# Kernel tuning notes

Hardware: AMD Instinct MI355X
Metric: run time of the kernel (lower is better)

Reference implementation:

```python
import jax, jax.numpy as jnp
import numpy as np

N, F_IN, F_OUT = 8192, 256, 128
ALPHA = 0.2  # LeakyReLU negative slope
NEG_INF = -9e15


def setup_inputs() -> dict:
    key = jax.random.key(0)
    k1, k2, k3, k4 = jax.random.split(key, 4)
    h = jax.random.normal(k1, (N, F_IN), dtype=jnp.float32)
    adj = jax.random.randint(k2, (N, N), 0, 2, dtype=jnp.int32)
    # Xavier-uniform-like init (gain=1.414)
    lim_w = 1.414 * np.sqrt(6.0 / (F_IN + F_OUT))
    W = jax.random.uniform(k3, (F_IN, F_OUT), dtype=jnp.float32, minval=-lim_w, maxval=lim_w)
    lim_a = 1.414 * np.sqrt(6.0 / (2 * F_OUT + 1))
    a = jax.random.uniform(k4, (2 * F_OUT, 1), dtype=jnp.float32, minval=-lim_a, maxval=lim_a)
    return {"h": h, "adj": adj, "W": W, "a": a}


def reference(h, adj, W, a):
    # Wh: [N, F_OUT]
    Wh = h @ W
    f_out = W.shape[1]
    # The torch code builds an [N, N, 2F] concat tensor; mathematically
    # e_ij = leakyrelu(a1 . Wh_i + a2 . Wh_j), so compute via two projections.
    a1 = a[:f_out, 0]   # [F_OUT]
    a2 = a[f_out:, 0]   # [F_OUT]
    f1 = Wh @ a1        # [N]
    f2 = Wh @ a2        # [N]
    e = jax.nn.leaky_relu(f1[:, None] + f2[None, :], negative_slope=ALPHA)  # [N, N]
    e = jnp.where(adj > 0, e, NEG_INF)
    attention = jax.nn.softmax(e, axis=1)  # [N, N]; dropout p=0 (eval mode)
    h_prime = attention @ Wh               # [N, F_OUT]
    return jax.nn.elu(h_prime)
```

## Files before the change

kernel.cpp:

```cpp
#include <hip/hip_runtime.h>
#include <hip/hip_bf16.h>
#include <math.h>

typedef short short8 __attribute__((ext_vector_type(8)));
typedef float f32x4 __attribute__((ext_vector_type(4)));
typedef int i32x4 __attribute__((ext_vector_type(4)));

#define NN 8192
#define FIN 256
#define FOUT 128
#define LRELU_A 0.2f
#define L2E 1.44269504088896f

__device__ __forceinline__ short f2bf(float x) {
    unsigned u = __builtin_bit_cast(unsigned, x);
    unsigned r = (u + 0x7FFFu + ((u >> 16) & 1u)) >> 16;
    return (short)r;
}

__device__ __forceinline__ short f2bf_fast(float x) {
    return __builtin_bit_cast(short, __float2bfloat16(x));
}

__global__ __launch_bounds__(256) void k_pack(const int* __restrict__ adj,
                                              unsigned* __restrict__ packed) {
    __shared__ unsigned char nib[2048];
    const int row = blockIdx.x;
    const int tid = threadIdx.x;
    const i32x4* base = (const i32x4*)(adj + (size_t)row * NN);
    #pragma unroll
    for (int q = 0; q < 8; ++q) {
        int idx = q * 256 + tid;
        i32x4 v = __builtin_nontemporal_load(base + idx);
        unsigned b = (unsigned)(v.x & 1)        | ((unsigned)(v.y & 1) << 1) |
                     ((unsigned)(v.z & 1) << 2) | ((unsigned)(v.w & 1) << 3);
        nib[idx] = (unsigned char)b;
    }
    __syncthreads();
    unsigned long long n8 = *(const unsigned long long*)&nib[tid * 8];
    unsigned w = 0;
    #pragma unroll
    for (int j = 0; j < 8; ++j)
        w |= ((unsigned)((n8 >> (8 * j)) & 0xFull)) << (4 * j);
    packed[(size_t)row * (NN / 32) + tid] = w;
}

__global__ __launch_bounds__(256) void k_wh(const float* __restrict__ h,
                                            const float* __restrict__ W,
                                            const float* __restrict__ a,
                                            short* __restrict__ WhT,
                                            float* __restrict__ f1,
                                            float* __restrict__ f2) {
    __shared__ float hs[8][FIN];
    const int tid = threadIdx.x;
    const int r0 = blockIdx.x * 8;
    #pragma unroll
    for (int i = 0; i < 2; ++i) {
        int f4 = tid + 256 * i;
        int row = f4 >> 6;
        int k4 = (f4 & 63) << 2;
        *(float4*)&hs[row][k4] = *(const float4*)(h + (size_t)(r0 + row) * FIN + k4);
    }
    __syncthreads();
    const int c4 = (tid & 31) * 4;
    const int row = tid >> 5;
    float acc0 = 0.f, acc1 = 0.f, acc2 = 0.f, acc3 = 0.f;
    #pragma unroll 4
    for (int k = 0; k < FIN; ++k) {
        float hv = hs[row][k];
        float4 w4 = *(const float4*)(W + (size_t)k * FOUT + c4);
        acc0 = fmaf(hv, w4.x, acc0);
        acc1 = fmaf(hv, w4.y, acc1);
        acc2 = fmaf(hv, w4.z, acc2);
        acc3 = fmaf(hv, w4.w, acc3);
    }
    const int wr = r0 + row;
    WhT[(size_t)(c4 + 0) * NN + wr] = f2bf(acc0);
    WhT[(size_t)(c4 + 1) * NN + wr] = f2bf(acc1);
    WhT[(size_t)(c4 + 2) * NN + wr] = f2bf(acc2);
    WhT[(size_t)(c4 + 3) * NN + wr] = f2bf(acc3);

    float4 a1v = *(const float4*)(a + c4);
    float4 a2v = *(const float4*)(a + FOUT + c4);
    float p1 = acc0 * a1v.x + acc1 * a1v.y + acc2 * a1v.z + acc3 * a1v.w;
    float p2 = acc0 * a2v.x + acc1 * a2v.y + acc2 * a2v.z + acc3 * a2v.w;
    #pragma unroll
    for (int m = 1; m <= 16; m <<= 1) {
        p1 += __shfl_xor(p1, m, 64);
        p2 += __shfl_xor(p2, m, 64);
    }
    if ((tid & 31) == 0) {
        f1[wr] = p1;
        f2[wr] = p2;
    }
}

__global__ __launch_bounds__(256) void k_gmax(const float* __restrict__ f2,
                                              float* __restrict__ gmax) {
    const int tid = threadIdx.x;
    float m = -1e30f;
    for (int i = tid; i < NN; i += 256) m = fmaxf(m, f2[i]);
    #pragma unroll
    for (int s = 1; s <= 32; s <<= 1) m = fmaxf(m, __shfl_xor(m, s, 64));
    __shared__ float red[4];
    if ((tid & 63) == 0) red[tid >> 6] = m;
    __syncthreads();
    if (tid == 0) gmax[0] = fmaxf(fmaxf(red[0], red[1]), fmaxf(red[2], red[3]));
}

__device__ __forceinline__ void gat_body(const short* __restrict__ lrd, unsigned m8,
                                         float4 fa, float4 fb,
                                         float c1, float c2,
                                         f32x4 acc[9], short8 ones) {
    short8 b0 = *(const short8*)(lrd + 0 * 1024);
    short8 b1 = *(const short8*)(lrd + 1 * 1024);
    short8 b2 = *(const short8*)(lrd + 2 * 1024);
    short8 b3 = *(const short8*)(lrd + 3 * 1024);
    short8 b4 = *(const short8*)(lrd + 4 * 1024);
    short8 b5 = *(const short8*)(lrd + 5 * 1024);
    short8 b6 = *(const short8*)(lrd + 6 * 1024);
    short8 b7 = *(const short8*)(lrd + 7 * 1024);

    float fv[8] = {fa.x, fa.y, fa.z, fa.w, fb.x, fb.y, fb.z, fb.w};
    short8 af;
    #pragma unroll
    for (int i = 0; i < 8; ++i) {
        float u = fv[i] + c1;
        float v = fmaf(LRELU_A, fv[i], c2);
        float p = __builtin_amdgcn_exp2f(fmaxf(u, v));
        p = (m8 & (1u << i)) ? p : 0.0f;
        af[i] = f2bf_fast(p);
    }
    acc[0] = __builtin_amdgcn_mfma_f32_16x16x32_bf16(af, b0, acc[0], 0, 0, 0);
    acc[1] = __builtin_amdgcn_mfma_f32_16x16x32_bf16(af, b1, acc[1], 0, 0, 0);
    acc[2] = __builtin_amdgcn_mfma_f32_16x16x32_bf16(af, b2, acc[2], 0, 0, 0);
    acc[3] = __builtin_amdgcn_mfma_f32_16x16x32_bf16(af, b3, acc[3], 0, 0, 0);
    acc[4] = __builtin_amdgcn_mfma_f32_16x16x32_bf16(af, b4, acc[4], 0, 0, 0);
    acc[5] = __builtin_amdgcn_mfma_f32_16x16x32_bf16(af, b5, acc[5], 0, 0, 0);
    acc[6] = __builtin_amdgcn_mfma_f32_16x16x32_bf16(af, b6, acc[6], 0, 0, 0);
    acc[7] = __builtin_amdgcn_mfma_f32_16x16x32_bf16(af, b7, acc[7], 0, 0, 0);
    acc[8] = __builtin_amdgcn_mfma_f32_16x16x32_bf16(af, ones, acc[8], 0, 0, 0);
}

#define GAT_STEP(KOFF, MC, LRD0, LRD1, BUFW)                                       \
    {                                                                              \
        const int koff_ = (KOFF);                                                  \
        float4 fa0 = *(const float4*)(lf2 + koff_);                                \
        float4 fb0 = *(const float4*)(lf2 + koff_ + 4);                            \
        float4 fa1 = *(const float4*)(lf2 + koff_ + 32);                           \
        float4 fb1 = *(const float4*)(lf2 + koff_ + 36);                           \
        unsigned m0 = (MC.x >> mshift) & 0xffu;                                    \
        unsigned m1 = (MC.y >> mshift) & 0xffu;                                    \
        const int kpm_ = (koff_ + 128 < kchunk) ? koff_ + 128 : 0;                 \
        MC = *(const uint2*)(pkrow + (kpm_ >> 5));                                 \
        const int kst_ = (koff_ + 64 < kchunk) ? koff_ + 64 : 0;                   \
        short8 r0 = *(const short8*)(g00 + kst_);                                  \
        short8 r1 = *(const short8*)(g01 + kst_);                                  \
        short8 r2 = *(const short8*)(g10 + kst_);                                  \
        short8 r3 = *(const short8*)(g11 + kst_);                                  \
        gat_body(LRD0, m0, fa0, fb0, c1, c2, acc, ones);                           \
        gat_body(LRD1, m1, fa1, fb1, c1, c2, acc, ones);                           \
        *(short8*)((BUFW) + d00) = r0;                                             \
        *(short8*)((BUFW) + d01) = r1;                                             \
        *(short8*)((BUFW) + d10) = r2;                                             \
        *(short8*)((BUFW) + d11) = r3;                                             \
        asm volatile("s_waitcnt lgkmcnt(0)" ::: "memory");                         \
        __builtin_amdgcn_s_barrier();                                              \
    }

__global__ __launch_bounds__(256, 4) void k_attn(const unsigned* __restrict__ packed,
                                                 const short* __restrict__ WhT,
                                                 const float* __restrict__ f1,
                                                 const float* __restrict__ f2,
                                                 const float* __restrict__ gmax,
                                                 float* __restrict__ numb,
                                                 float* __restrict__ denb,
                                                 int kchunk, int nsplit) {
    __shared__ __align__(16) short ldsW[2][8192];
    __shared__ __align__(16) float ldsF2[2048];
    const int tid = threadIdx.x;
    const int lane = tid & 63;
    const int wave = tid >> 6;
    const int split = blockIdx.x & (nsplit - 1);
    const int rt = blockIdx.x / nsplit;
    const int rowbase = rt * 64 + wave * 16;
    const int col = lane & 15;
    const int kg = lane >> 4;
    const int arow = rowbase + col;

    const float f1r = f1[arow];
    const float gm = gmax[0];
    const float t0v = f1r + gm;
    const float mhat = fmaxf(t0v, LRELU_A * t0v);
    const float mh2 = mhat * L2E;
    const float c1 = fmaf(f1r, L2E, -mh2);
    const float c2 = fmaf(LRELU_A * f1r, L2E, -mh2);

    const short8 ones = {0x3F80, 0x3F80, 0x3F80, 0x3F80,
                         0x3F80, 0x3F80, 0x3F80, 0x3F80};

    const int kbase0 = split * kchunk;
    const unsigned* pkrow = packed + (size_t)arow * (NN / 32) + (kbase0 >> 5);
    const int mshift = kg * 8;
    const float* lf2 = ldsF2 + kg * 8;

    const int srow = wave * 32 + (lane >> 2);
    const int sx = srow & 7;
    const short* gsb = WhT + (size_t)srow * NN + kbase0 + (lane & 3) * 8;
    const short* g00 = gsb;
    const short* g01 = gsb + 32;
    const short* g10 = gsb + (size_t)16 * NN;
    const short* g11 = gsb + (size_t)16 * NN + 32;
    const int d00 = srow * 64        + ((((lane & 3) + 0) ^ sx) * 8);
    const int d01 = srow * 64        + ((((lane & 3) + 4) ^ sx) * 8);
    const int d10 = (srow + 16) * 64 + ((((lane & 3) + 0) ^ sx) * 8);
    const int d11 = (srow + 16) * 64 + ((((lane & 3) + 4) ^ sx) * 8);
    short* buf0 = &ldsW[0][0];
    short* buf1 = &ldsW[1][0];

    const short* lrdE0 = &ldsW[0][col * 64 + ((kg ^ (col & 7)) * 8)];
    const short* lrdE1 = &ldsW[0][col * 64 + (((kg ^ (col & 7)) * 8) ^ 32)];
    const short* lrdO0 = lrdE0 + 8192;
    const short* lrdO1 = lrdE1 + 8192;

    f32x4 acc[9] = {};

    for (int i = tid * 4; i < kchunk; i += 1024) {
        float4 v = *(const float4*)(f2 + kbase0 + i);
        v.x *= L2E; v.y *= L2E; v.z *= L2E; v.w *= L2E;
        *(float4*)&ldsF2[i] = v;
    }
    {
        short8 r0 = *(const short8*)(g00);
        short8 r1 = *(const short8*)(g01);
        short8 r2 = *(const short8*)(g10);
        short8 r3 = *(const short8*)(g11);
        *(short8*)(buf0 + d00) = r0;
        *(short8*)(buf0 + d01) = r1;
        *(short8*)(buf0 + d10) = r2;
        *(short8*)(buf0 + d11) = r3;
    }
    uint2 mA = *(const uint2*)(pkrow);
    uint2 mB = *(const uint2*)(pkrow + 2);
    asm volatile("s_waitcnt lgkmcnt(0)" ::: "memory");
    __builtin_amdgcn_s_barrier();

    for (int koff = 0; koff < kchunk; koff += 128) {
        GAT_STEP(koff,      mA, lrdE0, lrdE1, buf1);
        GAT_STEP(koff + 64, mB, lrdO0, lrdO1, buf0);
    }

    const int rsub = (lane >> 4) * 4;
    if (col == 0) {
        #pragma unroll
        for (int r = 0; r < 4; ++r)
            denb[(size_t)split * NN + rowbase + rsub + r] = acc[8][r];
    }

    float* np = numb + ((size_t)split * NN + rowbase) * FOUT;
    #pragma unroll
    for (int t = 0; t < 8; ++t) {
        #pragma unroll
        for (int r = 0; r < 4; ++r) {
            np[(size_t)(rsub + r) * FOUT + t * 16 + col] = acc[t][r];
        }
    }
}

__global__ __launch_bounds__(256) void k_final(const float* __restrict__ numb,
                                               const float* __restrict__ denb,
                                               float* __restrict__ out,
                                               int splitk) {
    const int idx = blockIdx.x * 256 + threadIdx.x;
    const int row = idx >> 7;
    float s = 0.0f, d = 0.0f;
    for (int sp = 0; sp < splitk; ++sp) {
        s += numb[((size_t)sp * NN) * FOUT + idx];
        d += denb[(size_t)sp * NN + row];
    }
    float v = s / d;
    out[idx] = v > 0.0f ? v : expm1f(v);
}

extern "C" void kernel_launch(void* const* d_in, const int* in_sizes, int n_in,
                              void* d_out, int out_size, void* d_ws, size_t ws_size,
                              hipStream_t stream) {
    const float* h = (const float*)d_in[0];
    const int* adj = (const int*)d_in[1];
    const float* W = (const float*)d_in[2];
    const float* a = (const float*)d_in[3];
    float* out = (float*)d_out;

    char* ws = (char*)d_ws;
    size_t off = 0;
    auto alloc = [&](size_t nbytes) {
        char* p = ws + off;
        off = (off + nbytes + 255) & ~(size_t)255;
        return p;
    };
    short* WhT     = (short*)alloc((size_t)FOUT * NN * 2);
    float* f1      = (float*)alloc(NN * 4);
    float* f2      = (float*)alloc(NN * 4);
    float* gmx     = (float*)alloc(256);
    unsigned* pkd  = (unsigned*)alloc((size_t)NN * (NN / 32) * 4);

    int splitk = 8;
    while (splitk > 1 &&
           off + (size_t)splitk * ((size_t)NN * FOUT * 4 + NN * 4 + 512) > ws_size)
        splitk >>= 1;
    float* numb = (float*)alloc((size_t)splitk * NN * FOUT * 4);
    float* denb = (float*)alloc((size_t)splitk * NN * 4);
    const int kchunk = NN / splitk;

    k_wh<<<NN / 8, 256, 0, stream>>>(h, W, a, WhT, f1, f2);
    k_gmax<<<1, 256, 0, stream>>>(f2, gmx);
    k_pack<<<NN, 256, 0, stream>>>(adj, pkd);
    k_attn<<<(NN / 64) * splitk, 256, 0, stream>>>(pkd, WhT, f1, f2, gmx, numb, denb,
                                                   kchunk, splitk);
    k_final<<<NN * FOUT / 256, 256, 0, stream>>>(numb, denb, out, splitk);
}
```

Measured before the change: 132.8 us.

## Compute two 16-row tiles per wave in attention and fuse Wh with adjacency packing

Each wave in the attention kernel now handles 32 rows instead of 16, so every WhT B-fragment read from LDS feeds two sets of MFMAs. That halves LDS traffic and staging per output row, at the cost of doubled accumulator registers, which is why launch bounds drop from 4 to 2 blocks per CU. The Wh projection and the adjacency bit-packing are also merged into one prep kernel, removing a launch. The split-k floor is raised to 4.

```diff
diff --git a/kernel.cpp b/kernel.cpp
--- a/kernel.cpp
+++ b/kernel.cpp
@@ -22,38 +22,19 @@
     return __builtin_bit_cast(short, __float2bfloat16(x));
 }
 
-__global__ __launch_bounds__(256) void k_pack(const int* __restrict__ adj,
+__global__ __launch_bounds__(256) void k_prep(const float* __restrict__ h,
+                                              const float* __restrict__ W,
+                                              const float* __restrict__ a,
+                                              const int* __restrict__ adj,
+                                              short* __restrict__ WhT,
+                                              float* __restrict__ f1,
+                                              float* __restrict__ f2,
                                               unsigned* __restrict__ packed) {
+    __shared__ float hs[8][FIN];
     __shared__ unsigned char nib[2048];
-    const int row = blockIdx.x;
-    const int tid = threadIdx.x;
-    const i32x4* base = (const i32x4*)(adj + (size_t)row * NN);
-    #pragma unroll
-    for (int q = 0; q < 8; ++q) {
-        int idx = q * 256 + tid;
-        i32x4 v = __builtin_nontemporal_load(base + idx);
-        unsigned b = (unsigned)(v.x & 1)        | ((unsigned)(v.y & 1) << 1) |
-                     ((unsigned)(v.z & 1) << 2) | ((unsigned)(v.w & 1) << 3);
-        nib[idx] = (unsigned char)b;
-    }
-    __syncthreads();
-    unsigned long long n8 = *(const unsigned long long*)&nib[tid * 8];
-    unsigned w = 0;
-    #pragma unroll
-    for (int j = 0; j < 8; ++j)
-        w |= ((unsigned)((n8 >> (8 * j)) & 0xFull)) << (4 * j);
-    packed[(size_t)row * (NN / 32) + tid] = w;
-}
-
-__global__ __launch_bounds__(256) void k_wh(const float* __restrict__ h,
-                                            const float* __restrict__ W,
-                                            const float* __restrict__ a,
-                                            short* __restrict__ WhT,
-                                            float* __restrict__ f1,
-                                            float* __restrict__ f2) {
-    __shared__ float hs[8][FIN];
     const int tid = threadIdx.x;
     const int r0 = blockIdx.x * 8;
+
     #pragma unroll
     for (int i = 0; i < 2; ++i) {
         int f4 = tid + 256 * i;
@@ -93,6 +74,26 @@
         f1[wr] = p1;
         f2[wr] = p2;
     }
+
+    const i32x4* abase = (const i32x4*)(adj + (size_t)r0 * NN);
+    for (int r = 0; r < 8; ++r) {
+        #pragma unroll
+        for (int q = 0; q < 8; ++q) {
+            int idx = q * 256 + tid;
+            i32x4 v = __builtin_nontemporal_load(abase + (size_t)r * 2048 + idx);
+            unsigned b = (unsigned)(v.x & 1)        | ((unsigned)(v.y & 1) << 1) |
+                         ((unsigned)(v.z & 1) << 2) | ((unsigned)(v.w & 1) << 3);
+            nib[idx] = (unsigned char)b;
+        }
+        __syncthreads();
+        unsigned long long n8 = *(const unsigned long long*)&nib[tid * 8];
+        unsigned w = 0;
+        #pragma unroll
+        for (int j = 0; j < 8; ++j)
+            w |= ((unsigned)((n8 >> (8 * j)) & 0xFull)) << (4 * j);
+        packed[(size_t)(r0 + r) * (NN / 32) + tid] = w;
+        __syncthreads();
+    }
 }
 
 __global__ __launch_bounds__(256) void k_gmax(const float* __restrict__ f2,
@@ -108,10 +109,13 @@
     if (tid == 0) gmax[0] = fmaxf(fmaxf(red[0], red[1]), fmaxf(red[2], red[3]));
 }
 
-__device__ __forceinline__ void gat_body(const short* __restrict__ lrd, unsigned m8,
-                                         float4 fa, float4 fb,
-                                         float c1, float c2,
-                                         f32x4 acc[9], short8 ones) {
+__device__ __forceinline__ void gat_body2(const short* __restrict__ lrd,
+                                          unsigned m8L, unsigned m8H,
+                                          float4 fa, float4 fb,
+                                          float c1L, float c2L,
+                                          float c1H, float c2H,
+                                          f32x4 accL[9], f32x4 accH[9],
+                                          short8 ones) {
     short8 b0 = *(const short8*)(lrd + 0 * 1024);
     short8 b1 = *(const short8*)(lrd + 1 * 1024);
     short8 b2 = *(const short8*)(lrd + 2 * 1024);
@@ -122,44 +126,63 @@
     short8 b7 = *(const short8*)(lrd + 7 * 1024);
 
     float fv[8] = {fa.x, fa.y, fa.z, fa.w, fb.x, fb.y, fb.z, fb.w};
-    short8 af;
+    short8 afL, afH;
     #pragma unroll
     for (int i = 0; i < 8; ++i) {
-        float u = fv[i] + c1;
-        float v = fmaf(LRELU_A, fv[i], c2);
+        float u = fv[i] + c1L;
+        float v = fmaf(LRELU_A, fv[i], c2L);
         float p = __builtin_amdgcn_exp2f(fmaxf(u, v));
-        p = (m8 & (1u << i)) ? p : 0.0f;
-        af[i] = f2bf_fast(p);
-    }
-    acc[0] = __builtin_amdgcn_mfma_f32_16x16x32_bf16(af, b0, acc[0], 0, 0, 0);
-    acc[1] = __builtin_amdgcn_mfma_f32_16x16x32_bf16(af, b1, acc[1], 0, 0, 0);
-    acc[2] = __builtin_amdgcn_mfma_f32_16x16x32_bf16(af, b2, acc[2], 0, 0, 0);
-    acc[3] = __builtin_amdgcn_mfma_f32_16x16x32_bf16(af, b3, acc[3], 0, 0, 0);
-    acc[4] = __builtin_amdgcn_mfma_f32_16x16x32_bf16(af, b4, acc[4], 0, 0, 0);
-    acc[5] = __builtin_amdgcn_mfma_f32_16x16x32_bf16(af, b5, acc[5], 0, 0, 0);
-    acc[6] = __builtin_amdgcn_mfma_f32_16x16x32_bf16(af, b6, acc[6], 0, 0, 0);
-    acc[7] = __builtin_amdgcn_mfma_f32_16x16x32_bf16(af, b7, acc[7], 0, 0, 0);
-    acc[8] = __builtin_amdgcn_mfma_f32_16x16x32_bf16(af, ones, acc[8], 0, 0, 0);
-}
-
-#define GAT_STEP(KOFF, MC, LRD0, LRD1, BUFW)                                       \
+        afL[i] = f2bf_fast((m8L & (1u << i)) ? p : 0.0f);
+    }
+    accL[0] = __builtin_amdgcn_mfma_f32_16x16x32_bf16(afL, b0, accL[0], 0, 0, 0);
+    accL[1] = __builtin_amdgcn_mfma_f32_16x16x32_bf16(afL, b1, accL[1], 0, 0, 0);
+    accL[2] = __builtin_amdgcn_mfma_f32_16x16x32_bf16(afL, b2, accL[2], 0, 0, 0);
+    accL[3] = __builtin_amdgcn_mfma_f32_16x16x32_bf16(afL, b3, accL[3], 0, 0, 0);
+    accL[4] = __builtin_amdgcn_mfma_f32_16x16x32_bf16(afL, b4, accL[4], 0, 0, 0);
+    accL[5] = __builtin_amdgcn_mfma_f32_16x16x32_bf16(afL, b5, accL[5], 0, 0, 0);
+    accL[6] = __builtin_amdgcn_mfma_f32_16x16x32_bf16(afL, b6, accL[6], 0, 0, 0);
+    accL[7] = __builtin_amdgcn_mfma_f32_16x16x32_bf16(afL, b7, accL[7], 0, 0, 0);
+    accL[8] = __builtin_amdgcn_mfma_f32_16x16x32_bf16(afL, ones, accL[8], 0, 0, 0);
+
+    #pragma unroll
+    for (int i = 0; i < 8; ++i) {
+        float u = fv[i] + c1H;
+        float v = fmaf(LRELU_A, fv[i], c2H);
+        float p = __builtin_amdgcn_exp2f(fmaxf(u, v));
+        afH[i] = f2bf_fast((m8H & (1u << i)) ? p : 0.0f);
+    }
+    accH[0] = __builtin_amdgcn_mfma_f32_16x16x32_bf16(afH, b0, accH[0], 0, 0, 0);
+    accH[1] = __builtin_amdgcn_mfma_f32_16x16x32_bf16(afH, b1, accH[1], 0, 0, 0);
+    accH[2] = __builtin_amdgcn_mfma_f32_16x16x32_bf16(afH, b2, accH[2], 0, 0, 0);
+    accH[3] = __builtin_amdgcn_mfma_f32_16x16x32_bf16(afH, b3, accH[3], 0, 0, 0);
+    accH[4] = __builtin_amdgcn_mfma_f32_16x16x32_bf16(afH, b4, accH[4], 0, 0, 0);
+    accH[5] = __builtin_amdgcn_mfma_f32_16x16x32_bf16(afH, b5, accH[5], 0, 0, 0);
+    accH[6] = __builtin_amdgcn_mfma_f32_16x16x32_bf16(afH, b6, accH[6], 0, 0, 0);
+    accH[7] = __builtin_amdgcn_mfma_f32_16x16x32_bf16(afH, b7, accH[7], 0, 0, 0);
+    accH[8] = __builtin_amdgcn_mfma_f32_16x16x32_bf16(afH, ones, accH[8], 0, 0, 0);
+}
+
+#define GAT_STEP(KOFF, MCL, MCH, LRD0, LRD1, BUFW)                                 \
     {                                                                              \
         const int koff_ = (KOFF);                                                  \
         float4 fa0 = *(const float4*)(lf2 + koff_);                                \
         float4 fb0 = *(const float4*)(lf2 + koff_ + 4);                            \
         float4 fa1 = *(const float4*)(lf2 + koff_ + 32);                           \
         float4 fb1 = *(const float4*)(lf2 + koff_ + 36);                           \
-        unsigned m0 = (MC.x >> mshift) & 0xffu;                                    \
-        unsigned m1 = (MC.y >> mshift) & 0xffu;                                    \
+        unsigned m0L = (MCL.x >> mshift) & 0xffu;                                  \
+        unsigned m1L = (MCL.y >> mshift) & 0xffu;                                  \
+        unsigned m0H = (MCH.x >> mshift) & 0xffu;                                  \
+        unsigned m1H = (MCH.y >> mshift) & 0xffu;                                  \
         const int kpm_ = (koff_ + 128 < kchunk) ? koff_ + 128 : 0;                 \
-        MC = *(const uint2*)(pkrow + (kpm_ >> 5));                                 \
+        MCL = *(const uint2*)(pkrowL + (kpm_ >> 5));                               \
+        MCH = *(const uint2*)(pkrowH + (kpm_ >> 5));                               \
         const int kst_ = (koff_ + 64 < kchunk) ? koff_ + 64 : 0;                   \
         short8 r0 = *(const short8*)(g00 + kst_);                                  \
         short8 r1 = *(const short8*)(g01 + kst_);                                  \
         short8 r2 = *(const short8*)(g10 + kst_);                                  \
         short8 r3 = *(const short8*)(g11 + kst_);                                  \
-        gat_body(LRD0, m0, fa0, fb0, c1, c2, acc, ones);                           \
-        gat_body(LRD1, m1, fa1, fb1, c1, c2, acc, ones);                           \
+        gat_body2(LRD0, m0L, m0H, fa0, fb0, c1L, c2L, c1H, c2H, accL, accH, ones); \
+        gat_body2(LRD1, m1L, m1H, fa1, fb1, c1L, c2L, c1H, c2H, accL, accH, ones); \
         *(short8*)((BUFW) + d00) = r0;                                             \
         *(short8*)((BUFW) + d01) = r1;                                             \
         *(short8*)((BUFW) + d10) = r2;                                             \
@@ -168,7 +191,7 @@
         __builtin_amdgcn_s_barrier();                                              \
     }
 
-__global__ __launch_bounds__(256, 4) void k_attn(const unsigned* __restrict__ packed,
+__global__ __launch_bounds__(256, 2) void k_attn(const unsigned* __restrict__ packed,
                                                  const short* __restrict__ WhT,
                                                  const float* __restrict__ f1,
                                                  const float* __restrict__ f2,
@@ -183,24 +206,31 @@
     const int wave = tid >> 6;
     const int split = blockIdx.x & (nsplit - 1);
     const int rt = blockIdx.x / nsplit;
-    const int rowbase = rt * 64 + wave * 16;
+    const int rowbase = rt * 128 + wave * 32;
     const int col = lane & 15;
     const int kg = lane >> 4;
-    const int arow = rowbase + col;
-
-    const float f1r = f1[arow];
+    const int arowL = rowbase + col;
+    const int arowH = arowL + 16;
+
     const float gm = gmax[0];
-    const float t0v = f1r + gm;
-    const float mhat = fmaxf(t0v, LRELU_A * t0v);
-    const float mh2 = mhat * L2E;
-    const float c1 = fmaf(f1r, L2E, -mh2);
-    const float c2 = fmaf(LRELU_A * f1r, L2E, -mh2);
+    const float f1L = f1[arowL];
+    const float f1H = f1[arowH];
+    float t;
+    t = f1L + gm;
+    const float mhL = fmaxf(t, LRELU_A * t) * L2E;
+    const float c1L = fmaf(f1L, L2E, -mhL);
+    const float c2L = fmaf(LRELU_A * f1L, L2E, -mhL);
+    t = f1H + gm;
+    const float mhH = fmaxf(t, LRELU_A * t) * L2E;
+    const float c1H = fmaf(f1H, L2E, -mhH);
+    const float c2H = fmaf(LRELU_A * f1H, L2E, -mhH);
 
     const short8 ones = {0x3F80, 0x3F80, 0x3F80, 0x3F80,
                          0x3F80, 0x3F80, 0x3F80, 0x3F80};
 
     const int kbase0 = split * kchunk;
-    const unsigned* pkrow = packed + (size_t)arow * (NN / 32) + (kbase0 >> 5);
+    const unsigned* pkrowL = packed + (size_t)arowL * (NN / 32) + (kbase0 >> 5);
+    const unsigned* pkrowH = packed + (size_t)arowH * (NN / 32) + (kbase0 >> 5);
     const int mshift = kg * 8;
     const float* lf2 = ldsF2 + kg * 8;
 
@@ -223,7 +253,8 @@
     const short* lrdO0 = lrdE0 + 8192;
     const short* lrdO1 = lrdE1 + 8192;
 
-    f32x4 acc[9] = {};
+    f32x4 accL[9] = {};
+    f32x4 accH[9] = {};
 
     for (int i = tid * 4; i < kchunk; i += 1024) {
         float4 v = *(const float4*)(f2 + kbase0 + i);
@@ -240,29 +271,35 @@
         *(short8*)(buf0 + d10) = r2;
         *(short8*)(buf0 + d11) = r3;
     }
-    uint2 mA = *(const uint2*)(pkrow);
-    uint2 mB = *(const uint2*)(pkrow + 2);
+    uint2 mAL = *(const uint2*)(pkrowL);
+    uint2 mAH = *(const uint2*)(pkrowH);
+    uint2 mBL = *(const uint2*)(pkrowL + 2);
+    uint2 mBH = *(const uint2*)(pkrowH + 2);
     asm volatile("s_waitcnt lgkmcnt(0)" ::: "memory");
     __builtin_amdgcn_s_barrier();
 
     for (int koff = 0; koff < kchunk; koff += 128) {
-        GAT_STEP(koff,      mA, lrdE0, lrdE1, buf1);
-        GAT_STEP(koff + 64, mB, lrdO0, lrdO1, buf0);
+        GAT_STEP(koff,      mAL, mAH, lrdE0, lrdE1, buf1);
+        GAT_STEP(koff + 64, mBL, mBH, lrdO0, lrdO1, buf0);
     }
 
     const int rsub = (lane >> 4) * 4;
     if (col == 0) {
         #pragma unroll
-        for (int r = 0; r < 4; ++r)
-            denb[(size_t)split * NN + rowbase + rsub + r] = acc[8][r];
-    }
-
-    float* np = numb + ((size_t)split * NN + rowbase) * FOUT;
-    #pragma unroll
-    for (int t = 0; t < 8; ++t) {
+        for (int r = 0; r < 4; ++r) {
+            denb[(size_t)split * NN + rowbase + rsub + r] = accL[8][r];
+            denb[(size_t)split * NN + rowbase + 16 + rsub + r] = accH[8][r];
+        }
+    }
+
+    float* npL = numb + ((size_t)split * NN + rowbase) * FOUT;
+    float* npH = npL + (size_t)16 * FOUT;
+    #pragma unroll
+    for (int tcol = 0; tcol < 8; ++tcol) {
         #pragma unroll
         for (int r = 0; r < 4; ++r) {
-            np[(size_t)(rsub + r) * FOUT + t * 16 + col] = acc[t][r];
+            npL[(size_t)(rsub + r) * FOUT + tcol * 16 + col] = accL[tcol][r];
+            npH[(size_t)(rsub + r) * FOUT + tcol * 16 + col] = accH[tcol][r];
         }
     }
 }
@@ -305,17 +342,16 @@
     unsigned* pkd  = (unsigned*)alloc((size_t)NN * (NN / 32) * 4);
 
     int splitk = 8;
-    while (splitk > 1 &&
+    while (splitk > 4 &&
            off + (size_t)splitk * ((size_t)NN * FOUT * 4 + NN * 4 + 512) > ws_size)
         splitk >>= 1;
     float* numb = (float*)alloc((size_t)splitk * NN * FOUT * 4);
     float* denb = (float*)alloc((size_t)splitk * NN * 4);
     const int kchunk = NN / splitk;
 
-    k_wh<<<NN / 8, 256, 0, stream>>>(h, W, a, WhT, f1, f2);
+    k_prep<<<NN / 8, 256, 0, stream>>>(h, W, a, adj, WhT, f1, f2, pkd);
     k_gmax<<<1, 256, 0, stream>>>(f2, gmx);
-    k_pack<<<NN, 256, 0, stream>>>(adj, pkd);
-    k_attn<<<(NN / 64) * splitk, 256, 0, stream>>>(pkd, WhT, f1, f2, gmx, numb, denb,
-                                                   kchunk, splitk);
+    k_attn<<<(NN / 128) * splitk, 256, 0, stream>>>(pkd, WhT, f1, f2, gmx, numb, denb,
+                                                    kchunk, splitk);
     k_final<<<NN * FOUT / 256, 256, 0, stream>>>(numb, denb, out, splitk);
 }
```

Measured after the change: 137.8 us. +3.8%, slower.
